# Performance work log

Hardware: AMD Instinct MI355X
Metric: run time of the kernel (lower is better)

Reference implementation:

```python
import jax, jax.numpy as jnp
import numpy as np

N_NODES = 100000
N_EDGES = 3200000
D_FEAT = 64


def setup_inputs() -> dict:
    key = jax.random.key(0)
    k1, k2, k3 = jax.random.split(key, 3)
    x = jax.random.normal(k1, (N_NODES, D_FEAT), dtype=jnp.float32)
    up_index = jax.random.randint(k2, (2, N_EDGES), 0, N_NODES, dtype=jnp.int64)
    down_index = jax.random.randint(k3, (2, N_EDGES), 0, N_NODES, dtype=jnp.int64)
    return {"x": x, "up_index": up_index, "down_index": down_index}


def _propagate(x, edge_index, num_nodes):
    # flow = 'source_to_target': (i, j) = (1, 0)
    # __lift__: gather x along node_dim=-2 at source indices (row j=0)
    msg = x[edge_index[0]]                      # [E, D]  message_up(x_j) = x_j
    # aggregate 'add': scatter-add messages to target indices (row i=1)
    return jax.ops.segment_sum(msg, edge_index[1], num_segments=num_nodes)  # [N, D]


def reference(x, up_index, down_index):
    up_out = _propagate(x, up_index, x.shape[0])
    down_out = _propagate(x, down_index, x.shape[0])
    # update: combine up and down aggregations (identity update -> sum)
    return up_out + down_out
```

## Files before the change

kernel.cpp:

```cpp
#include <hip/hip_runtime.h>


static constexpr int D = 64;
static constexpr int Q = 16;
static constexpr int NPB = 64;
static constexpr int NPB_SHIFT = 6;
static constexpr int CHUNK = 8192;
static constexpr int CH = 4096;
static constexpr int SLABS = 16;
static constexpr int NBIN = NPB * SLABS;

__global__ void detect_idx_dtype(const int* __restrict__ w, int* __restrict__ flag) {
    int tid = threadIdx.x;
    int v = w[2 * tid + 1];
    unsigned long long m = __ballot(v != 0);
    if (tid == 0) *flag = (m == 0ULL) ? 1 : 0;
}

__device__ __forceinline__ int load_idx(const void* idx, long long i, int is64) {
    return is64 ? (int)((const long long*)idx)[i] : ((const int*)idx)[i];
}

__global__ __launch_bounds__(256) void bucket_hist_kernel(
        const void* __restrict__ up, const void* __restrict__ down,
        int* __restrict__ bcounts, const int* __restrict__ flag, int E, int NB) {
    extern __shared__ int lcnt[];
    const int is64 = *flag;
    for (int i = threadIdx.x; i < NB; i += blockDim.x) lcnt[i] = 0;
    __syncthreads();
    const long long total = 2LL * E;
    const long long stride = (long long)gridDim.x * blockDim.x;
    for (long long e = (long long)blockIdx.x * blockDim.x + threadIdx.x;
         e < total; e += stride) {
        const void* idx = up; long long ee = e;
        if (ee >= E) { idx = down; ee -= E; }
        int dst = load_idx(idx, E + ee, is64);
        atomicAdd(&lcnt[dst >> NPB_SHIFT], 1);
    }
    __syncthreads();
    for (int i = threadIdx.x; i < NB; i += blockDim.x)
        if (lcnt[i]) atomicAdd(&bcounts[i], lcnt[i]);
}

__global__ __launch_bounds__(1024) void scan_kernel(
        const int* __restrict__ counts, int* __restrict__ offsets,
        int* __restrict__ cursors, int NB) {
    __shared__ int sums[1024];
    const int tid = threadIdx.x;
    const int chunk = (NB + 1023) / 1024;
    const int start = tid * chunk;
    const int end = min(start + chunk, NB);
    int s = 0;
    for (int i = start; i < end; i++) s += counts[i];
    sums[tid] = s;
    __syncthreads();
    for (int off = 1; off < 1024; off <<= 1) {
        int t = (tid >= off) ? sums[tid - off] : 0;
        __syncthreads();
        sums[tid] += t;
        __syncthreads();
    }
    int run = (tid == 0) ? 0 : sums[tid - 1];
    for (int i = start; i < end; i++) {
        offsets[i] = run;
        cursors[i] = run;
        run += counts[i];
    }
    if (tid == 1023) offsets[NB] = run;
}

__global__ __launch_bounds__(256) void bucket_scatter_kernel(
        const void* __restrict__ up, const void* __restrict__ down,
        int* __restrict__ gcursor, unsigned* __restrict__ packed,
        const int* __restrict__ flag, int E, int NB) {
    extern __shared__ int lds[];
    int* cnt = lds;
    int* base = lds + NB;
    const int is64 = *flag;
    const long long total = 2LL * E;
    const long long cs = (long long)blockIdx.x * CHUNK;
    if (cs >= total) return;
    const long long ce = min(total, cs + (long long)CHUNK);

    for (int i = threadIdx.x; i < NB; i += blockDim.x) cnt[i] = 0;
    __syncthreads();
    for (long long e = cs + threadIdx.x; e < ce; e += blockDim.x) {
        const void* idx = up; long long ee = e;
        if (ee >= E) { idx = down; ee -= E; }
        int dst = load_idx(idx, E + ee, is64);
        atomicAdd(&cnt[dst >> NPB_SHIFT], 1);
    }
    __syncthreads();
    for (int i = threadIdx.x; i < NB; i += blockDim.x) {
        int c = cnt[i];
        base[i] = c ? atomicAdd(&gcursor[i], c) : 0;
        cnt[i] = 0;
    }
    __syncthreads();
    for (long long e = cs + threadIdx.x; e < ce; e += blockDim.x) {
        const void* idx = up; long long ee = e;
        if (ee >= E) { idx = down; ee -= E; }
        int src = load_idx(idx, ee, is64);
        int dst = load_idx(idx, E + ee, is64);
        int b = dst >> NPB_SHIFT;
        int pos = base[b] + atomicAdd(&cnt[b], 1);
        packed[pos] = ((unsigned)src << NPB_SHIFT) | (unsigned)(dst & (NPB - 1));
    }
}

__global__ __launch_bounds__(256) void bucket_gather_kernel(
        const float* __restrict__ x, const int* __restrict__ offsets,
        const unsigned* __restrict__ packed, float* __restrict__ out,
        int N, int sshift) {
    __shared__ unsigned sorted[CH];
    __shared__ int cnt[NBIN];
    __shared__ int binoff[NBIN + 1];
    __shared__ int cursor[NBIN];
    __shared__ int wsum[4];

    const int b = blockIdx.x;
    const int tid = threadIdx.x;
    const int g = tid >> 4;
    const int q = tid & 15;
    const int lane = tid & 63;
    const int wv = tid >> 6;
    const int beg = offsets[b], end = offsets[b + 1];

    float4 acc[4];
    acc[0] = acc[1] = acc[2] = acc[3] = make_float4(0.f, 0.f, 0.f, 0.f);

    for (int cs = beg; cs < end; cs += CH) {
        const int m = min(CH, end - cs);
        #pragma unroll
        for (int i = 0; i < NBIN / 256; i++) cnt[tid + 256 * i] = 0;
        __syncthreads();
        for (int i = tid; i < m; i += 256) {
            unsigned p = packed[cs + i];
            int key = ((p & (NPB - 1)) << 4) | (int)((p >> NPB_SHIFT) >> sshift);
            atomicAdd(&cnt[key], 1);
        }
        __syncthreads();
        {
            int b0 = cnt[4 * tid], b1 = cnt[4 * tid + 1];
            int b2 = cnt[4 * tid + 2], b3 = cnt[4 * tid + 3];
            int tsum = b0 + b1 + b2 + b3;
            int inc = tsum;
            #pragma unroll
            for (int off = 1; off < 64; off <<= 1) {
                int t = __shfl_up(inc, off, 64);
                if (lane >= off) inc += t;
            }
            if (lane == 63) wsum[wv] = inc;
            __syncthreads();
            int wbase = 0;
            #pragma unroll
            for (int w = 0; w < 4; w++) wbase += (w < wv) ? wsum[w] : 0;
            int excl = wbase + inc - tsum;
            binoff[4 * tid] = excl; cursor[4 * tid] = excl; excl += b0;
            binoff[4 * tid + 1] = excl; cursor[4 * tid + 1] = excl; excl += b1;
            binoff[4 * tid + 2] = excl; cursor[4 * tid + 2] = excl; excl += b2;
            binoff[4 * tid + 3] = excl; cursor[4 * tid + 3] = excl; excl += b3;
            if (tid == 255) binoff[NBIN] = excl;
        }
        __syncthreads();
        for (int i = tid; i < m; i += 256) {
            unsigned p = packed[cs + i];
            int key = ((p & (NPB - 1)) << 4) | (int)((p >> NPB_SHIFT) >> sshift);
            int pos = atomicAdd(&cursor[key], 1);
            sorted[pos] = p;
        }
        __syncthreads();
        #pragma unroll
        for (int j = 0; j < 4; j++) {
            const int dl = 4 * g + j;
            const int rb = binoff[dl << 4], re = binoff[(dl + 1) << 4];
            int e = rb;
            for (; e + 3 < re; e += 4) {
                unsigned p0 = sorted[e], p1 = sorted[e + 1];
                unsigned p2 = sorted[e + 2], p3 = sorted[e + 3];
                const float4 v0 = *(const float4*)(x + ((long long)(p0 >> NPB_SHIFT)) * D + q * 4);
                const float4 v1 = *(const float4*)(x + ((long long)(p1 >> NPB_SHIFT)) * D + q * 4);
                const float4 v2 = *(const float4*)(x + ((long long)(p2 >> NPB_SHIFT)) * D + q * 4);
                const float4 v3 = *(const float4*)(x + ((long long)(p3 >> NPB_SHIFT)) * D + q * 4);
                acc[j].x += (v0.x + v1.x) + (v2.x + v3.x);
                acc[j].y += (v0.y + v1.y) + (v2.y + v3.y);
                acc[j].z += (v0.z + v1.z) + (v2.z + v3.z);
                acc[j].w += (v0.w + v1.w) + (v2.w + v3.w);
            }
            for (; e < re; e++) {
                unsigned p = sorted[e];
                const float4 v = *(const float4*)(x + ((long long)(p >> NPB_SHIFT)) * D + q * 4);
                acc[j].x += v.x; acc[j].y += v.y; acc[j].z += v.z; acc[j].w += v.w;
            }
        }
        __syncthreads();
    }

    const int node0 = b * NPB;
    #pragma unroll
    for (int j = 0; j < 4; j++) {
        const int node = node0 + 4 * g + j;
        if (node < N)
            *(float4*)(out + (long long)node * D + q * 4) = acc[j];
    }
}

__global__ __launch_bounds__(256) void scatter_add_kernel(
        const float* __restrict__ x, const void* __restrict__ up_idx,
        const void* __restrict__ down_idx, float* __restrict__ out,
        const int* __restrict__ dtype_flag, int num_edges) {
    const int is64 = *dtype_flag;
    const long long total = 2LL * num_edges * Q;
    const long long stride = (long long)gridDim.x * blockDim.x;
    for (long long t = (long long)blockIdx.x * blockDim.x + threadIdx.x;
         t < total; t += stride) {
        const int quad = (int)(t & (Q - 1));
        long long eg = t >> 4;
        const void* idx = up_idx;
        if (eg >= num_edges) { idx = down_idx; eg -= num_edges; }
        int src = load_idx(idx, eg, is64);
        int dst = load_idx(idx, num_edges + eg, is64);
        const float4 v = *(const float4*)(x + (long long)src * D + quad * 4);
        float* o = out + (long long)dst * D + quad * 4;
        unsafeAtomicAdd(o + 0, v.x);
        unsafeAtomicAdd(o + 1, v.y);
        unsafeAtomicAdd(o + 2, v.z);
        unsafeAtomicAdd(o + 3, v.w);
    }
}

extern "C" void kernel_launch(void* const* d_in, const int* in_sizes, int n_in,
                              void* d_out, int out_size, void* d_ws, size_t ws_size,
                              hipStream_t stream) {
    const float* x = (const float*)d_in[0];
    const void* up_idx = d_in[1];
    const void* down_idx = d_in[2];
    float* out = (float*)d_out;

    const int E = in_sizes[1] / 2;
    const int N = out_size / D;
    const int NB = (N + NPB - 1) / NPB;
    const long long Etot = 2LL * E;

    int sshift = 0;
    while (((unsigned)(N - 1) >> sshift) >= SLABS) sshift++;

    int* ws_i = (int*)d_ws;
    int* flag = ws_i;
    int* counts = ws_i + 64;
    int* offsets = counts + NB;
    int* cursors = offsets + NB + 15;
    unsigned* packed = (unsigned*)(cursors + NB);
    const size_t ws_need = (size_t)(64 + 3LL * NB + 16 + Etot) * 4 + 64;

    detect_idx_dtype<<<1, 64, 0, stream>>>((const int*)up_idx, flag);

    if (ws_size >= ws_need && N <= (1 << 25) && Etot < (1LL << 31)) {
        hipMemsetAsync(counts, 0, (size_t)NB * sizeof(int), stream);
        bucket_hist_kernel<<<1024, 256, NB * sizeof(int), stream>>>(
            up_idx, down_idx, counts, flag, E, NB);
        scan_kernel<<<1, 1024, 0, stream>>>(counts, offsets, cursors, NB);
        const int sblocks = (int)((Etot + CHUNK - 1) / CHUNK);
        bucket_scatter_kernel<<<sblocks, 256, 2 * NB * sizeof(int), stream>>>(
            up_idx, down_idx, cursors, packed, flag, E, NB);
        bucket_gather_kernel<<<NB, 256, 0, stream>>>(x, offsets, packed, out, N, sshift);
    } else {
        hipMemsetAsync(d_out, 0, (size_t)out_size * sizeof(float), stream);
        scatter_add_kernel<<<8192, 256, 0, stream>>>(x, up_idx, down_idx, out, flag, E);
    }
}
```

Measured before the change: 501.2 us.

## Replace histogram+scan with fixed-capacity buckets and overflow list; shrink node buckets

Removes the separate histogram and scan kernels by giving each destination bucket a fixed-capacity slot region, with padded global cursors to avoid atomic contention and an overflow list handled by an atomic cleanup kernel. Buckets shrink to 32 nodes with 32 source slabs, and the gather iterates slab-major so concurrent threads read nearby source rows. This trades one full pass over the index arrays for workspace over-allocation and a possible atomic fallback path, and doubles the number of gather blocks.

```diff
diff --git a/kernel.cpp b/kernel.cpp
--- a/kernel.cpp
+++ b/kernel.cpp
@@ -3,12 +3,13 @@
 
 static constexpr int D = 64;
 static constexpr int Q = 16;
-static constexpr int NPB = 64;
-static constexpr int NPB_SHIFT = 6;
+static constexpr int NPB = 32;
+static constexpr int NPB_SHIFT = 5;
+static constexpr int SLABS = 32;
+static constexpr int NBIN = NPB * SLABS;
 static constexpr int CHUNK = 8192;
-static constexpr int CH = 4096;
-static constexpr int SLABS = 16;
-static constexpr int NBIN = NPB * SLABS;
+static constexpr int CH = 2048;
+static constexpr int CURPAD = 16;
 
 __global__ void detect_idx_dtype(const int* __restrict__ w, int* __restrict__ flag) {
     int tid = threadIdx.x;
@@ -21,57 +22,10 @@
     return is64 ? (int)((const long long*)idx)[i] : ((const int*)idx)[i];
 }
 
-__global__ __launch_bounds__(256) void bucket_hist_kernel(
-        const void* __restrict__ up, const void* __restrict__ down,
-        int* __restrict__ bcounts, const int* __restrict__ flag, int E, int NB) {
-    extern __shared__ int lcnt[];
-    const int is64 = *flag;
-    for (int i = threadIdx.x; i < NB; i += blockDim.x) lcnt[i] = 0;
-    __syncthreads();
-    const long long total = 2LL * E;
-    const long long stride = (long long)gridDim.x * blockDim.x;
-    for (long long e = (long long)blockIdx.x * blockDim.x + threadIdx.x;
-         e < total; e += stride) {
-        const void* idx = up; long long ee = e;
-        if (ee >= E) { idx = down; ee -= E; }
-        int dst = load_idx(idx, E + ee, is64);
-        atomicAdd(&lcnt[dst >> NPB_SHIFT], 1);
-    }
-    __syncthreads();
-    for (int i = threadIdx.x; i < NB; i += blockDim.x)
-        if (lcnt[i]) atomicAdd(&bcounts[i], lcnt[i]);
-}
-
-__global__ __launch_bounds__(1024) void scan_kernel(
-        const int* __restrict__ counts, int* __restrict__ offsets,
-        int* __restrict__ cursors, int NB) {
-    __shared__ int sums[1024];
-    const int tid = threadIdx.x;
-    const int chunk = (NB + 1023) / 1024;
-    const int start = tid * chunk;
-    const int end = min(start + chunk, NB);
-    int s = 0;
-    for (int i = start; i < end; i++) s += counts[i];
-    sums[tid] = s;
-    __syncthreads();
-    for (int off = 1; off < 1024; off <<= 1) {
-        int t = (tid >= off) ? sums[tid - off] : 0;
-        __syncthreads();
-        sums[tid] += t;
-        __syncthreads();
-    }
-    int run = (tid == 0) ? 0 : sums[tid - 1];
-    for (int i = start; i < end; i++) {
-        offsets[i] = run;
-        cursors[i] = run;
-        run += counts[i];
-    }
-    if (tid == 1023) offsets[NB] = run;
-}
-
 __global__ __launch_bounds__(256) void bucket_scatter_kernel(
         const void* __restrict__ up, const void* __restrict__ down,
-        int* __restrict__ gcursor, unsigned* __restrict__ packed,
+        int* __restrict__ gcursor, unsigned* __restrict__ packed, int cap,
+        int* __restrict__ ovf_cnt, int2* __restrict__ ovf_list, int ovf_cap,
         const int* __restrict__ flag, int E, int NB) {
     extern __shared__ int lds[];
     int* cnt = lds;
@@ -82,36 +36,42 @@
     if (cs >= total) return;
     const long long ce = min(total, cs + (long long)CHUNK);
 
-    for (int i = threadIdx.x; i < NB; i += blockDim.x) cnt[i] = 0;
+    for (int i = threadIdx.x; i < NB; i += 256) cnt[i] = 0;
     __syncthreads();
-    for (long long e = cs + threadIdx.x; e < ce; e += blockDim.x) {
+    for (long long e = cs + threadIdx.x; e < ce; e += 256) {
         const void* idx = up; long long ee = e;
         if (ee >= E) { idx = down; ee -= E; }
         int dst = load_idx(idx, E + ee, is64);
         atomicAdd(&cnt[dst >> NPB_SHIFT], 1);
     }
     __syncthreads();
-    for (int i = threadIdx.x; i < NB; i += blockDim.x) {
+    for (int i = threadIdx.x; i < NB; i += 256) {
         int c = cnt[i];
-        base[i] = c ? atomicAdd(&gcursor[i], c) : 0;
+        base[i] = c ? atomicAdd(&gcursor[i * CURPAD], c) : 0;
         cnt[i] = 0;
     }
     __syncthreads();
-    for (long long e = cs + threadIdx.x; e < ce; e += blockDim.x) {
+    for (long long e = cs + threadIdx.x; e < ce; e += 256) {
         const void* idx = up; long long ee = e;
         if (ee >= E) { idx = down; ee -= E; }
         int src = load_idx(idx, ee, is64);
         int dst = load_idx(idx, E + ee, is64);
         int b = dst >> NPB_SHIFT;
         int pos = base[b] + atomicAdd(&cnt[b], 1);
-        packed[pos] = ((unsigned)src << NPB_SHIFT) | (unsigned)(dst & (NPB - 1));
+        if (pos < cap) {
+            packed[(long long)b * cap + pos] =
+                ((unsigned)src << NPB_SHIFT) | (unsigned)(dst & (NPB - 1));
+        } else {
+            int o = atomicAdd(ovf_cnt, 1);
+            if (o < ovf_cap) ovf_list[o] = make_int2(src, dst);
+        }
     }
 }
 
 __global__ __launch_bounds__(256) void bucket_gather_kernel(
-        const float* __restrict__ x, const int* __restrict__ offsets,
-        const unsigned* __restrict__ packed, float* __restrict__ out,
-        int N, int sshift) {
+        const float* __restrict__ x, const int* __restrict__ gcursor,
+        const unsigned* __restrict__ packed, int cap,
+        float* __restrict__ out, int N, int sshift) {
     __shared__ unsigned sorted[CH];
     __shared__ int cnt[NBIN];
     __shared__ int binoff[NBIN + 1];
@@ -124,19 +84,20 @@
     const int q = tid & 15;
     const int lane = tid & 63;
     const int wv = tid >> 6;
-    const int beg = offsets[b], end = offsets[b + 1];
-
-    float4 acc[4];
-    acc[0] = acc[1] = acc[2] = acc[3] = make_float4(0.f, 0.f, 0.f, 0.f);
-
-    for (int cs = beg; cs < end; cs += CH) {
-        const int m = min(CH, end - cs);
+    const long long pbase = (long long)b * cap;
+    const int total = min(gcursor[b * CURPAD], cap);
+
+    float4 acc[2];
+    acc[0] = acc[1] = make_float4(0.f, 0.f, 0.f, 0.f);
+
+    for (int cs0 = 0; cs0 < total; cs0 += CH) {
+        const int m = min(CH, total - cs0);
         #pragma unroll
         for (int i = 0; i < NBIN / 256; i++) cnt[tid + 256 * i] = 0;
         __syncthreads();
         for (int i = tid; i < m; i += 256) {
-            unsigned p = packed[cs + i];
-            int key = ((p & (NPB - 1)) << 4) | (int)((p >> NPB_SHIFT) >> sshift);
+            unsigned p = packed[pbase + cs0 + i];
+            int key = ((int)((p >> NPB_SHIFT) >> sshift) << NPB_SHIFT) | (int)(p & (NPB - 1));
             atomicAdd(&cnt[key], 1);
         }
         __syncthreads();
@@ -164,33 +125,35 @@
         }
         __syncthreads();
         for (int i = tid; i < m; i += 256) {
-            unsigned p = packed[cs + i];
-            int key = ((p & (NPB - 1)) << 4) | (int)((p >> NPB_SHIFT) >> sshift);
+            unsigned p = packed[pbase + cs0 + i];
+            int key = ((int)((p >> NPB_SHIFT) >> sshift) << NPB_SHIFT) | (int)(p & (NPB - 1));
             int pos = atomicAdd(&cursor[key], 1);
             sorted[pos] = p;
         }
         __syncthreads();
-        #pragma unroll
-        for (int j = 0; j < 4; j++) {
-            const int dl = 4 * g + j;
-            const int rb = binoff[dl << 4], re = binoff[(dl + 1) << 4];
-            int e = rb;
-            for (; e + 3 < re; e += 4) {
-                unsigned p0 = sorted[e], p1 = sorted[e + 1];
-                unsigned p2 = sorted[e + 2], p3 = sorted[e + 3];
-                const float4 v0 = *(const float4*)(x + ((long long)(p0 >> NPB_SHIFT)) * D + q * 4);
-                const float4 v1 = *(const float4*)(x + ((long long)(p1 >> NPB_SHIFT)) * D + q * 4);
-                const float4 v2 = *(const float4*)(x + ((long long)(p2 >> NPB_SHIFT)) * D + q * 4);
-                const float4 v3 = *(const float4*)(x + ((long long)(p3 >> NPB_SHIFT)) * D + q * 4);
-                acc[j].x += (v0.x + v1.x) + (v2.x + v3.x);
-                acc[j].y += (v0.y + v1.y) + (v2.y + v3.y);
-                acc[j].z += (v0.z + v1.z) + (v2.z + v3.z);
-                acc[j].w += (v0.w + v1.w) + (v2.w + v3.w);
-            }
-            for (; e < re; e++) {
-                unsigned p = sorted[e];
-                const float4 v = *(const float4*)(x + ((long long)(p >> NPB_SHIFT)) * D + q * 4);
-                acc[j].x += v.x; acc[j].y += v.y; acc[j].z += v.z; acc[j].w += v.w;
+        for (int s = 0; s < SLABS; s++) {
+            #pragma unroll
+            for (int j = 0; j < 2; j++) {
+                const int bin = (s << NPB_SHIFT) | (2 * g + j);
+                const int rb = binoff[bin], re = binoff[bin + 1];
+                int e = rb;
+                for (; e + 3 < re; e += 4) {
+                    unsigned p0 = sorted[e], p1 = sorted[e + 1];
+                    unsigned p2 = sorted[e + 2], p3 = sorted[e + 3];
+                    const float4 v0 = *(const float4*)(x + ((long long)(p0 >> NPB_SHIFT)) * D + q * 4);
+                    const float4 v1 = *(const float4*)(x + ((long long)(p1 >> NPB_SHIFT)) * D + q * 4);
+                    const float4 v2 = *(const float4*)(x + ((long long)(p2 >> NPB_SHIFT)) * D + q * 4);
+                    const float4 v3 = *(const float4*)(x + ((long long)(p3 >> NPB_SHIFT)) * D + q * 4);
+                    acc[j].x += (v0.x + v1.x) + (v2.x + v3.x);
+                    acc[j].y += (v0.y + v1.y) + (v2.y + v3.y);
+                    acc[j].z += (v0.z + v1.z) + (v2.z + v3.z);
+                    acc[j].w += (v0.w + v1.w) + (v2.w + v3.w);
+                }
+                for (; e < re; e++) {
+                    unsigned p = sorted[e];
+                    const float4 v = *(const float4*)(x + ((long long)(p >> NPB_SHIFT)) * D + q * 4);
+                    acc[j].x += v.x; acc[j].y += v.y; acc[j].z += v.z; acc[j].w += v.w;
+                }
             }
         }
         __syncthreads();
@@ -198,10 +161,30 @@
 
     const int node0 = b * NPB;
     #pragma unroll
-    for (int j = 0; j < 4; j++) {
-        const int node = node0 + 4 * g + j;
+    for (int j = 0; j < 2; j++) {
+        const int node = node0 + 2 * g + j;
         if (node < N)
             *(float4*)(out + (long long)node * D + q * 4) = acc[j];
+    }
+}
+
+__global__ __launch_bounds__(256) void cleanup_kernel(
+        const float* __restrict__ x, const int* __restrict__ ovf_cnt,
+        const int2* __restrict__ list, int ovf_cap, float* __restrict__ out) {
+    const int cnt = min(*ovf_cnt, ovf_cap);
+    const long long totalq = (long long)cnt * Q;
+    const long long stride = (long long)gridDim.x * blockDim.x;
+    for (long long t = (long long)blockIdx.x * blockDim.x + threadIdx.x;
+         t < totalq; t += stride) {
+        const int e = (int)(t >> 4);
+        const int q = (int)(t & 15);
+        const int2 sd = list[e];
+        const float4 v = *(const float4*)(x + (long long)sd.x * D + q * 4);
+        float* o = out + (long long)sd.y * D + q * 4;
+        unsafeAtomicAdd(o + 0, v.x);
+        unsafeAtomicAdd(o + 1, v.y);
+        unsafeAtomicAdd(o + 2, v.z);
+        unsafeAtomicAdd(o + 3, v.w);
     }
 }
 
@@ -247,23 +230,35 @@
 
     int* ws_i = (int*)d_ws;
     int* flag = ws_i;
-    int* counts = ws_i + 64;
-    int* offsets = counts + NB;
-    int* cursors = offsets + NB + 15;
-    unsigned* packed = (unsigned*)(cursors + NB);
-    const size_t ws_need = (size_t)(64 + 3LL * NB + 16 + Etot) * 4 + 64;
+    int* gcursor = ws_i + 64;
+    int* ovf_cnt = gcursor + (long long)NB * CURPAD;
+    const long long fixed = 64 + (long long)NB * CURPAD + 16;
+    const long long avail = (long long)(ws_size / 4) - fixed;
+    const long long capmin = (Etot + NB - 1) / NB;
+
+    int ovf_cap = 1 << 20;
+    long long cap = 0;
+    for (;;) {
+        cap = (avail - 2LL * ovf_cap) / NB;
+        if (cap >= capmin || ovf_cap <= (1 << 14)) break;
+        ovf_cap >>= 1;
+    }
+    if (cap > 8192) cap = 8192;
+    int2* ovf_list = (int2*)(ovf_cnt + 16);
+    unsigned* packed = (unsigned*)((int*)ovf_list + 2LL * ovf_cap);
 
     detect_idx_dtype<<<1, 64, 0, stream>>>((const int*)up_idx, flag);
 
-    if (ws_size >= ws_need && N <= (1 << 25) && Etot < (1LL << 31)) {
-        hipMemsetAsync(counts, 0, (size_t)NB * sizeof(int), stream);
-        bucket_hist_kernel<<<1024, 256, NB * sizeof(int), stream>>>(
-            up_idx, down_idx, counts, flag, E, NB);
-        scan_kernel<<<1, 1024, 0, stream>>>(counts, offsets, cursors, NB);
+    if (cap >= capmin && cap >= 1 && E >= 64 && N >= 1 &&
+        N <= (1 << 23) && Etot < (1LL << 31)) {
+        hipMemsetAsync(gcursor, 0, ((size_t)NB * CURPAD + 16) * sizeof(int), stream);
         const int sblocks = (int)((Etot + CHUNK - 1) / CHUNK);
         bucket_scatter_kernel<<<sblocks, 256, 2 * NB * sizeof(int), stream>>>(
-            up_idx, down_idx, cursors, packed, flag, E, NB);
-        bucket_gather_kernel<<<NB, 256, 0, stream>>>(x, offsets, packed, out, N, sshift);
+            up_idx, down_idx, gcursor, packed, (int)cap,
+            ovf_cnt, ovf_list, ovf_cap, flag, E, NB);
+        bucket_gather_kernel<<<NB, 256, 0, stream>>>(
+            x, gcursor, packed, (int)cap, out, N, sshift);
+        cleanup_kernel<<<256, 256, 0, stream>>>(x, ovf_cnt, ovf_list, ovf_cap, out);
     } else {
         hipMemsetAsync(d_out, 0, (size_t)out_size * sizeof(float), stream);
         scatter_add_kernel<<<8192, 256, 0, stream>>>(x, up_idx, down_idx, out, flag, E);
```

After: 522.3 us. 4.2% more time.

## Split bucket scatter into two-level radix passes by superbucket then fine bucket

Applied to the files above, without the earlier changes.

Replaces the single scatter pass into ~1563 fine buckets with two passes: pass A partitions edges into at most 64 superbuckets (32 fine buckets each, padded global cursors), and pass B refines each superbucket into fine buckets, using a binary search over superbucket offsets. The goal is fewer scattered global writes per block and less LDS and global-atomic pressure than one wide scatter. The gather kernel's in-block sort key is reordered to slab-major so that the per-node loop walks source-range slabs in order. This adds an extra full pass over the edge records and a second Etot-sized buffer, and the fast path now requires N <= 2^17.

```diff
diff --git a/kernel.cpp b/kernel.cpp
--- a/kernel.cpp
+++ b/kernel.cpp
@@ -5,10 +5,14 @@
 static constexpr int Q = 16;
 static constexpr int NPB = 64;
 static constexpr int NPB_SHIFT = 6;
-static constexpr int CHUNK = 8192;
-static constexpr int CH = 4096;
+static constexpr int FPSB = 32;
+static constexpr int NPSB_SHIFT = 11;
+static constexpr int SB_MASK = 2047;
 static constexpr int SLABS = 16;
 static constexpr int NBIN = NPB * SLABS;
+static constexpr int CHUNK = 16384;
+static constexpr int CH = 4096;
+static constexpr int CURPAD = 16;
 
 __global__ void detect_idx_dtype(const int* __restrict__ w, int* __restrict__ flag) {
     int tid = threadIdx.x;
@@ -21,12 +25,12 @@
     return is64 ? (int)((const long long*)idx)[i] : ((const int*)idx)[i];
 }
 
-__global__ __launch_bounds__(256) void bucket_hist_kernel(
+__global__ __launch_bounds__(256) void hist_kernel(
         const void* __restrict__ up, const void* __restrict__ down,
-        int* __restrict__ bcounts, const int* __restrict__ flag, int E, int NB) {
+        int* __restrict__ fineCnt, const int* __restrict__ flag, int E, int NB) {
     extern __shared__ int lcnt[];
     const int is64 = *flag;
-    for (int i = threadIdx.x; i < NB; i += blockDim.x) lcnt[i] = 0;
+    for (int i = threadIdx.x; i < NB; i += 256) lcnt[i] = 0;
     __syncthreads();
     const long long total = 2LL * E;
     const long long stride = (long long)gridDim.x * blockDim.x;
@@ -38,20 +42,21 @@
         atomicAdd(&lcnt[dst >> NPB_SHIFT], 1);
     }
     __syncthreads();
-    for (int i = threadIdx.x; i < NB; i += blockDim.x)
-        if (lcnt[i]) atomicAdd(&bcounts[i], lcnt[i]);
+    for (int i = threadIdx.x; i < NB; i += 256)
+        if (lcnt[i]) atomicAdd(&fineCnt[i], lcnt[i]);
 }
 
 __global__ __launch_bounds__(1024) void scan_kernel(
-        const int* __restrict__ counts, int* __restrict__ offsets,
-        int* __restrict__ cursors, int NB) {
+        const int* __restrict__ fineCnt, int* __restrict__ fineOff,
+        int* __restrict__ fineCur, int* __restrict__ sbOff,
+        int* __restrict__ sbCur, int NB, int SB) {
     __shared__ int sums[1024];
     const int tid = threadIdx.x;
     const int chunk = (NB + 1023) / 1024;
     const int start = tid * chunk;
     const int end = min(start + chunk, NB);
     int s = 0;
-    for (int i = start; i < end; i++) s += counts[i];
+    for (int i = start; i < end; i++) s += fineCnt[i];
     sums[tid] = s;
     __syncthreads();
     for (int off = 1; off < 1024; off <<= 1) {
@@ -62,55 +67,109 @@
     }
     int run = (tid == 0) ? 0 : sums[tid - 1];
     for (int i = start; i < end; i++) {
-        offsets[i] = run;
-        cursors[i] = run;
-        run += counts[i];
-    }
-    if (tid == 1023) offsets[NB] = run;
-}
-
-__global__ __launch_bounds__(256) void bucket_scatter_kernel(
+        fineOff[i] = run;
+        fineCur[i] = run;
+        run += fineCnt[i];
+    }
+    if (tid == 1023) fineOff[NB] = run;
+    __syncthreads();
+    if (tid <= SB) {
+        int v = fineOff[min(tid * FPSB, NB)];
+        sbOff[tid] = v;
+        if (tid < SB) sbCur[tid * CURPAD] = v;
+    }
+}
+
+__global__ __launch_bounds__(256) void passA_kernel(
         const void* __restrict__ up, const void* __restrict__ down,
-        int* __restrict__ gcursor, unsigned* __restrict__ packed,
-        const int* __restrict__ flag, int E, int NB) {
-    extern __shared__ int lds[];
-    int* cnt = lds;
-    int* base = lds + NB;
+        int* __restrict__ sbCur, unsigned* __restrict__ recA,
+        const int* __restrict__ flag, int E, int SB) {
+    __shared__ int cnt[64];
+    __shared__ int base[64];
     const int is64 = *flag;
     const long long total = 2LL * E;
     const long long cs = (long long)blockIdx.x * CHUNK;
     if (cs >= total) return;
     const long long ce = min(total, cs + (long long)CHUNK);
 
-    for (int i = threadIdx.x; i < NB; i += blockDim.x) cnt[i] = 0;
-    __syncthreads();
-    for (long long e = cs + threadIdx.x; e < ce; e += blockDim.x) {
+    if (threadIdx.x < 64) cnt[threadIdx.x] = 0;
+    __syncthreads();
+    for (long long e = cs + threadIdx.x; e < ce; e += 256) {
         const void* idx = up; long long ee = e;
         if (ee >= E) { idx = down; ee -= E; }
         int dst = load_idx(idx, E + ee, is64);
-        atomicAdd(&cnt[dst >> NPB_SHIFT], 1);
-    }
-    __syncthreads();
-    for (int i = threadIdx.x; i < NB; i += blockDim.x) {
-        int c = cnt[i];
-        base[i] = c ? atomicAdd(&gcursor[i], c) : 0;
+        atomicAdd(&cnt[dst >> NPSB_SHIFT], 1);
+    }
+    __syncthreads();
+    if (threadIdx.x < 64) {
+        int i = threadIdx.x;
+        int c = (i < SB) ? cnt[i] : 0;
+        base[i] = c ? atomicAdd(&sbCur[i * CURPAD], c) : 0;
         cnt[i] = 0;
     }
     __syncthreads();
-    for (long long e = cs + threadIdx.x; e < ce; e += blockDim.x) {
+    for (long long e = cs + threadIdx.x; e < ce; e += 256) {
         const void* idx = up; long long ee = e;
         if (ee >= E) { idx = down; ee -= E; }
         int src = load_idx(idx, ee, is64);
         int dst = load_idx(idx, E + ee, is64);
-        int b = dst >> NPB_SHIFT;
-        int pos = base[b] + atomicAdd(&cnt[b], 1);
-        packed[pos] = ((unsigned)src << NPB_SHIFT) | (unsigned)(dst & (NPB - 1));
+        int k = dst >> NPSB_SHIFT;
+        int pos = base[k] + atomicAdd(&cnt[k], 1);
+        recA[pos] = ((unsigned)src << NPSB_SHIFT) | (unsigned)(dst & SB_MASK);
+    }
+}
+
+__global__ __launch_bounds__(256) void passB_kernel(
+        const unsigned* __restrict__ recA, const int* __restrict__ sbOffG,
+        int* __restrict__ fineCur, unsigned* __restrict__ recB,
+        long long total, int NB, int SB) {
+    extern __shared__ int lds[];
+    int* sbOff = lds;
+    int* cnt = lds + SB + 1;
+    int* base = cnt + NB;
+
+    const long long cs = (long long)blockIdx.x * CHUNK;
+    if (cs >= total) return;
+    const long long ce = min(total, cs + (long long)CHUNK);
+
+    for (int i = threadIdx.x; i <= SB; i += 256) sbOff[i] = sbOffG[i];
+    for (int i = threadIdx.x; i < NB; i += 256) cnt[i] = 0;
+    __syncthreads();
+
+    for (long long i = cs + threadIdx.x; i < ce; i += 256) {
+        int lo = 0, hi = SB - 1;
+        while (lo < hi) {
+            int mid = (lo + hi + 1) >> 1;
+            if ((long long)sbOff[mid] <= i) lo = mid; else hi = mid - 1;
+        }
+        unsigned r = recA[i];
+        int f = lo * FPSB + (int)((r & SB_MASK) >> NPB_SHIFT);
+        atomicAdd(&cnt[f], 1);
+    }
+    __syncthreads();
+    for (int i = threadIdx.x; i < NB; i += 256) {
+        int c = cnt[i];
+        base[i] = c ? atomicAdd(&fineCur[i], c) : 0;
+        cnt[i] = 0;
+    }
+    __syncthreads();
+    for (long long i = cs + threadIdx.x; i < ce; i += 256) {
+        int lo = 0, hi = SB - 1;
+        while (lo < hi) {
+            int mid = (lo + hi + 1) >> 1;
+            if ((long long)sbOff[mid] <= i) lo = mid; else hi = mid - 1;
+        }
+        unsigned r = recA[i];
+        int dl = (int)(r & SB_MASK);
+        int f = lo * FPSB + (dl >> NPB_SHIFT);
+        int pos = base[f] + atomicAdd(&cnt[f], 1);
+        recB[pos] = ((r >> NPSB_SHIFT) << NPB_SHIFT) | (unsigned)(dl & (NPB - 1));
     }
 }
 
 __global__ __launch_bounds__(256) void bucket_gather_kernel(
-        const float* __restrict__ x, const int* __restrict__ offsets,
-        const unsigned* __restrict__ packed, float* __restrict__ out,
+        const float* __restrict__ x, const int* __restrict__ fineOff,
+        const unsigned* __restrict__ recB, float* __restrict__ out,
         int N, int sshift) {
     __shared__ unsigned sorted[CH];
     __shared__ int cnt[NBIN];
@@ -124,7 +183,7 @@
     const int q = tid & 15;
     const int lane = tid & 63;
     const int wv = tid >> 6;
-    const int beg = offsets[b], end = offsets[b + 1];
+    const int beg = fineOff[b], end = fineOff[b + 1];
 
     float4 acc[4];
     acc[0] = acc[1] = acc[2] = acc[3] = make_float4(0.f, 0.f, 0.f, 0.f);
@@ -135,8 +194,8 @@
         for (int i = 0; i < NBIN / 256; i++) cnt[tid + 256 * i] = 0;
         __syncthreads();
         for (int i = tid; i < m; i += 256) {
-            unsigned p = packed[cs + i];
-            int key = ((p & (NPB - 1)) << 4) | (int)((p >> NPB_SHIFT) >> sshift);
+            unsigned p = recB[cs + i];
+            int key = ((int)((p >> NPB_SHIFT) >> sshift) << NPB_SHIFT) | (int)(p & (NPB - 1));
             atomicAdd(&cnt[key], 1);
         }
         __syncthreads();
@@ -164,33 +223,35 @@
         }
         __syncthreads();
         for (int i = tid; i < m; i += 256) {
-            unsigned p = packed[cs + i];
-            int key = ((p & (NPB - 1)) << 4) | (int)((p >> NPB_SHIFT) >> sshift);
+            unsigned p = recB[cs + i];
+            int key = ((int)((p >> NPB_SHIFT) >> sshift) << NPB_SHIFT) | (int)(p & (NPB - 1));
             int pos = atomicAdd(&cursor[key], 1);
             sorted[pos] = p;
         }
         __syncthreads();
-        #pragma unroll
-        for (int j = 0; j < 4; j++) {
-            const int dl = 4 * g + j;
-            const int rb = binoff[dl << 4], re = binoff[(dl + 1) << 4];
-            int e = rb;
-            for (; e + 3 < re; e += 4) {
-                unsigned p0 = sorted[e], p1 = sorted[e + 1];
-                unsigned p2 = sorted[e + 2], p3 = sorted[e + 3];
-                const float4 v0 = *(const float4*)(x + ((long long)(p0 >> NPB_SHIFT)) * D + q * 4);
-                const float4 v1 = *(const float4*)(x + ((long long)(p1 >> NPB_SHIFT)) * D + q * 4);
-                const float4 v2 = *(const float4*)(x + ((long long)(p2 >> NPB_SHIFT)) * D + q * 4);
-                const float4 v3 = *(const float4*)(x + ((long long)(p3 >> NPB_SHIFT)) * D + q * 4);
-                acc[j].x += (v0.x + v1.x) + (v2.x + v3.x);
-                acc[j].y += (v0.y + v1.y) + (v2.y + v3.y);
-                acc[j].z += (v0.z + v1.z) + (v2.z + v3.z);
-                acc[j].w += (v0.w + v1.w) + (v2.w + v3.w);
-            }
-            for (; e < re; e++) {
-                unsigned p = sorted[e];
-                const float4 v = *(const float4*)(x + ((long long)(p >> NPB_SHIFT)) * D + q * 4);
-                acc[j].x += v.x; acc[j].y += v.y; acc[j].z += v.z; acc[j].w += v.w;
+        for (int s = 0; s < SLABS; s++) {
+            #pragma unroll
+            for (int j = 0; j < 4; j++) {
+                const int bin = (s << NPB_SHIFT) | (4 * g + j);
+                const int rb = binoff[bin], re = binoff[bin + 1];
+                int e = rb;
+                for (; e + 3 < re; e += 4) {
+                    unsigned p0 = sorted[e], p1 = sorted[e + 1];
+                    unsigned p2 = sorted[e + 2], p3 = sorted[e + 3];
+                    const float4 v0 = *(const float4*)(x + ((long long)(p0 >> NPB_SHIFT)) * D + q * 4);
+                    const float4 v1 = *(const float4*)(x + ((long long)(p1 >> NPB_SHIFT)) * D + q * 4);
+                    const float4 v2 = *(const float4*)(x + ((long long)(p2 >> NPB_SHIFT)) * D + q * 4);
+                    const float4 v3 = *(const float4*)(x + ((long long)(p3 >> NPB_SHIFT)) * D + q * 4);
+                    acc[j].x += (v0.x + v1.x) + (v2.x + v3.x);
+                    acc[j].y += (v0.y + v1.y) + (v2.y + v3.y);
+                    acc[j].z += (v0.z + v1.z) + (v2.z + v3.z);
+                    acc[j].w += (v0.w + v1.w) + (v2.w + v3.w);
+                }
+                for (; e < re; e++) {
+                    unsigned p = sorted[e];
+                    const float4 v = *(const float4*)(x + ((long long)(p >> NPB_SHIFT)) * D + q * 4);
+                    acc[j].x += v.x; acc[j].y += v.y; acc[j].z += v.z; acc[j].w += v.w;
+                }
             }
         }
         __syncthreads();
@@ -240,6 +301,7 @@
     const int E = in_sizes[1] / 2;
     const int N = out_size / D;
     const int NB = (N + NPB - 1) / NPB;
+    const int SB = (NB + FPSB - 1) / FPSB;
     const long long Etot = 2LL * E;
 
     int sshift = 0;
@@ -247,23 +309,30 @@
 
     int* ws_i = (int*)d_ws;
     int* flag = ws_i;
-    int* counts = ws_i + 64;
-    int* offsets = counts + NB;
-    int* cursors = offsets + NB + 15;
-    unsigned* packed = (unsigned*)(cursors + NB);
-    const size_t ws_need = (size_t)(64 + 3LL * NB + 16 + Etot) * 4 + 64;
+    int* fineCnt = ws_i + 64;
+    int* fineOff = fineCnt + NB;
+    int* fineCur = fineOff + NB + 1 + 15;
+    int* sbOff = fineCur + NB;
+    int* sbCur = sbOff + SB + 1 + 15;
+    unsigned* recA = (unsigned*)(sbCur + (long long)SB * CURPAD);
+    unsigned* recB = recA + Etot;
+    const size_t ws_need = (size_t)(64 + 3LL * NB + 16 + SB + 16 +
+                                    (long long)SB * CURPAD + 2LL * Etot) * 4 + 64;
 
     detect_idx_dtype<<<1, 64, 0, stream>>>((const int*)up_idx, flag);
 
-    if (ws_size >= ws_need && N <= (1 << 25) && Etot < (1LL << 31)) {
-        hipMemsetAsync(counts, 0, (size_t)NB * sizeof(int), stream);
-        bucket_hist_kernel<<<1024, 256, NB * sizeof(int), stream>>>(
-            up_idx, down_idx, counts, flag, E, NB);
-        scan_kernel<<<1, 1024, 0, stream>>>(counts, offsets, cursors, NB);
-        const int sblocks = (int)((Etot + CHUNK - 1) / CHUNK);
-        bucket_scatter_kernel<<<sblocks, 256, 2 * NB * sizeof(int), stream>>>(
-            up_idx, down_idx, cursors, packed, flag, E, NB);
-        bucket_gather_kernel<<<NB, 256, 0, stream>>>(x, offsets, packed, out, N, sshift);
+    if (ws_size >= ws_need && E >= 64 && N >= 1 &&
+        N <= (1 << 17) && SB <= 64 && Etot < (1LL << 31)) {
+        hipMemsetAsync(fineCnt, 0, (size_t)NB * sizeof(int), stream);
+        hist_kernel<<<1024, 256, NB * sizeof(int), stream>>>(
+            up_idx, down_idx, fineCnt, flag, E, NB);
+        scan_kernel<<<1, 1024, 0, stream>>>(fineCnt, fineOff, fineCur, sbOff, sbCur, NB, SB);
+        const int pblocks = (int)((Etot + CHUNK - 1) / CHUNK);
+        passA_kernel<<<pblocks, 256, 0, stream>>>(
+            up_idx, down_idx, sbCur, recA, flag, E, SB);
+        passB_kernel<<<pblocks, 256, (SB + 1 + 2 * NB) * sizeof(int), stream>>>(
+            recA, sbOff, fineCur, recB, Etot, NB, SB);
+        bucket_gather_kernel<<<NB, 256, 0, stream>>>(x, fineOff, recB, out, N, sshift);
     } else {
         hipMemsetAsync(d_out, 0, (size_t)out_size * sizeof(float), stream);
         scatter_add_kernel<<<8192, 256, 0, stream>>>(x, up_idx, down_idx, out, flag, E);
```

Measured after the change: 504.2 us. Within noise of the previous version (+0.6%).
